# Performance work log

Hardware: AMD Instinct MI355X
Metric: run time of the kernel (lower is better)

The kernel has to match this reference:

```python
import jax, jax.numpy as jnp
import numpy as np

N_NODES = 100000
N_EDGES = 3200000
IN_DIM, HID_DIM, OUT_DIM = 128, 64, 2


def setup_inputs() -> dict:
    key = jax.random.key(0)
    k1, k2, k3, k4 = jax.random.split(key, 4)
    x = jax.random.normal(k1, (N_NODES, IN_DIM), dtype=jnp.float32)
    edge_index = jax.random.randint(k2, (2, N_EDGES), 0, N_NODES, dtype=jnp.int64)
    # GCNConv weights (glorot-style scale) and zero biases
    W1 = jax.random.normal(k3, (IN_DIM, HID_DIM), dtype=jnp.float32) / np.sqrt(IN_DIM)
    b1 = jnp.zeros((HID_DIM,), dtype=jnp.float32)
    W2 = jax.random.normal(k4, (HID_DIM, OUT_DIM), dtype=jnp.float32) / np.sqrt(HID_DIM)
    b2 = jnp.zeros((OUT_DIM,), dtype=jnp.float32)
    return {"x": x, "edge_index": edge_index, "W1": W1, "b1": b1, "W2": W2, "b2": b2}


def _gcn_norm(edge_index, num_nodes):
    # PyG GCNConv default: add self-loops, symmetric normalization deg^-1/2.
    loops = jnp.arange(num_nodes, dtype=edge_index.dtype)
    src = jnp.concatenate([edge_index[0], loops])  # [E+N]
    dst = jnp.concatenate([edge_index[1], loops])  # [E+N]
    deg = jax.ops.segment_sum(jnp.ones_like(dst, dtype=jnp.float32), dst,
                              num_segments=num_nodes)  # in-degree incl. self-loop
    dinv = jnp.where(deg > 0, jax.lax.rsqrt(deg), 0.0)
    norm = dinv[src] * dinv[dst]  # [E+N]
    return src, dst, norm


def _gcn_conv(h, W, b, src, dst, norm, num_nodes):
    h = h @ W                              # dense transform first (smaller dim)
    msg = h[src] * norm[:, None]           # gather + scale: [E+N, d]
    out = jax.ops.segment_sum(msg, dst, num_segments=num_nodes)  # scatter-add
    return out + b


def reference(x, edge_index, W1, b1, W2, b2):
    n = x.shape[0]
    src, dst, norm = _gcn_norm(edge_index, n)
    h = _gcn_conv(x, W1, b1, src, dst, norm, n)
    h = jax.nn.relu(h)
    return _gcn_conv(h, W2, b2, src, dst, norm, n)
```

## Files before the change

kernel.cpp:

```cpp
#include <hip/hip_runtime.h>
#include <hip/hip_bf16.h>


#define N_NODES 100000
#define IN_DIM 128
#define HID_DIM 64
#define OUT_DIM 2
#define NB 391
#define BCAP 12288
#define CROUNDS 12
#define CHUNK 8192

typedef short bf16x8 __attribute__((ext_vector_type(8)));
typedef float f32x4 __attribute__((ext_vector_type(4)));

__device__ __forceinline__ unsigned short f2bf(float x) {
    unsigned int u = __float_as_uint(x);
    unsigned int r = (u + 0x7FFFu + ((u >> 16) & 1u)) >> 16;
    return (unsigned short)r;
}
__device__ __forceinline__ float bflo(unsigned int u) { return __uint_as_float(u << 16); }
__device__ __forceinline__ float bfhi(unsigned int u) { return __uint_as_float(u & 0xFFFF0000u); }
__device__ __forceinline__ float4 unplo(uint4 r) {
    return make_float4(bflo(r.x), bflo(r.y), bflo(r.z), bflo(r.w));
}
__device__ __forceinline__ float4 unphi(uint4 r) {
    return make_float4(bfhi(r.x), bfhi(r.y), bfhi(r.z), bfhi(r.w));
}
__device__ __forceinline__ float4 f4add(float4 a, float4 v) {
    return make_float4(a.x + v.x, a.y + v.y, a.z + v.z, a.w + v.w);
}
__device__ __forceinline__ float4 f4fma(float m, float4 v, float4 a) {
    return make_float4(fmaf(m, v.x, a.x), fmaf(m, v.y, a.y),
                       fmaf(m, v.z, a.z), fmaf(m, v.w, a.w));
}
__device__ __forceinline__ int wave_incl_scan(int v, int laneid) {
#pragma unroll
    for (int off = 1; off < 64; off <<= 1) {
        int u = __shfl_up(v, off);
        if (laneid >= off) v += u;
    }
    return v;
}

__global__ __launch_bounds__(512) void part_kernel(const int* __restrict__ ei,
                                                   int* __restrict__ gCursor,
                                                   int* __restrict__ part, int E) {
    __shared__ int hist[512], lrow[512], gbase[512], lcur[512];
    __shared__ int lpk[CHUNK];
    __shared__ short lbkt[CHUNK];
    __shared__ int wsum[8], wofs[8];
    const int t = threadIdx.x;
    const int lane = t & 63, wv = t >> 6;
    const int base = blockIdx.x * CHUNK;
    const int cntC = min(CHUNK, E - base);

    hist[t] = 0;
    __syncthreads();

    int s[16], d[16];
    bool val[16];
    if (base + CHUNK <= E) {
#pragma unroll
        for (int i = 0; i < 4; ++i) {
            int4 sv = ((const int4*)(ei + base))[t + i * 512];
            int4 dv = ((const int4*)(ei + E + base))[t + i * 512];
            s[i * 4 + 0] = sv.x; s[i * 4 + 1] = sv.y; s[i * 4 + 2] = sv.z; s[i * 4 + 3] = sv.w;
            d[i * 4 + 0] = dv.x; d[i * 4 + 1] = dv.y; d[i * 4 + 2] = dv.z; d[i * 4 + 3] = dv.w;
            val[i * 4 + 0] = val[i * 4 + 1] = val[i * 4 + 2] = val[i * 4 + 3] = true;
        }
    } else {
#pragma unroll
        for (int i = 0; i < 16; ++i) {
            int e = base + t + i * 512;
            val[i] = (e < E);
            if (val[i]) {
                s[i] = ei[e];
                d[i] = ei[E + e];
            }
        }
    }
#pragma unroll
    for (int i = 0; i < 16; ++i)
        if (val[i]) atomicAdd(&hist[d[i] >> 8], 1);
    __syncthreads();

    int v = hist[t];
    int inc = wave_incl_scan(v, lane);
    if (lane == 63) wsum[wv] = inc;
    __syncthreads();
    if (t < 64) {
        int w = (t < 8) ? wsum[t] : 0;
        int wi = wave_incl_scan(w, t);
        if (t < 8) wofs[t] = wi - w;
    }
    __syncthreads();
    int excl = inc - v + wofs[wv];
    if (t < NB && v > 0) {
        int old = atomicAdd(&gCursor[t], v);
        gbase[t] = t * BCAP + old;
    }
    lcur[t] = excl;
    lrow[t] = excl;
    __syncthreads();

#pragma unroll
    for (int i = 0; i < 16; ++i) {
        if (val[i]) {
            int b = d[i] >> 8;
            int pos = atomicAdd(&lcur[b], 1);
            lpk[pos] = s[i] | ((d[i] & 255) << 20);
            lbkt[pos] = (short)b;
        }
    }
    __syncthreads();

    for (int i = t; i < cntC; i += 512) {
        int b = lbkt[i];
        int g = gbase[b] + (i - lrow[b]);
        if (g < (b + 1) * BCAP)
            part[g] = lpk[i];
    }
}

__global__ __launch_bounds__(1024) void csr_kernel(const int* __restrict__ part,
                                                   const int* __restrict__ gCursor,
                                                   int* __restrict__ cnt,
                                                   float* __restrict__ dinv,
                                                   int* __restrict__ rowptr,
                                                   int* __restrict__ csr_src, int n) {
    __shared__ int wcnt[16][256];
    __shared__ int wsum[4], wofs[4];
    const int b = blockIdx.x, t = threadIdx.x;
    const int lane = t & 63, wv = t >> 6;
    const int start = b * BCAP;
    const int count = min(gCursor[b], BCAP);

    for (int i = t; i < 16 * 256; i += 1024) ((int*)wcnt)[i] = 0;
    __syncthreads();

    int pk[CROUNDS];
    bool val[CROUNDS];
#pragma unroll
    for (int k = 0; k < CROUNDS; ++k) {
        int i = t + k * 1024;
        val[k] = (i < count);
        pk[k] = val[k] ? part[start + i] : 0;
        if (val[k]) atomicAdd(&wcnt[wv][(pk[k] >> 20) & 255], 1);
    }
    __syncthreads();

    int v = 0;
    if (t < 256) {
        int sum = 0;
#pragma unroll
        for (int w = 0; w < 16; ++w) sum += wcnt[w][t];
        v = sum;
    }
    int inc = 0;
    if (t < 256) {
        inc = wave_incl_scan(v, lane);
        if (lane == 63) wsum[wv] = inc;
    }
    __syncthreads();
    if (t < 64) {
        int w = (t < 4) ? wsum[t] : 0;
        int wi = wave_incl_scan(w, t);
        if (t < 4) wofs[t] = wi - w;
    }
    __syncthreads();
    if (t < 256) {
        int excl = inc - v + wofs[wv];
        int node = (b << 8) + t;
        if (node < n) {
            cnt[node] = v;
            dinv[node] = rsqrtf((float)v + 1.0f);
            rowptr[node] = start + excl;
        }
        int run = excl;
#pragma unroll
        for (int w = 0; w < 16; ++w) {
            int c = wcnt[w][t];
            wcnt[w][t] = run;
            run += c;
        }
    }
    __syncthreads();

#pragma unroll
    for (int k = 0; k < CROUNDS; ++k) {
        if (val[k]) {
            int pos = atomicAdd(&wcnt[wv][(pk[k] >> 20) & 255], 1);
            csr_src[start + pos] = pk[k] & 0xFFFFF;
        }
    }
}

__global__ __launch_bounds__(256) void gemm1_kernel(const float* __restrict__ x,
                                                    const float* __restrict__ W1,
                                                    const float* __restrict__ dinv,
                                                    unsigned short* __restrict__ hsb, int n) {
    __shared__ unsigned short sX[64 * 136];
    __shared__ unsigned short sW[64 * 136];
    const int tid = threadIdx.x;
    const int rbase = blockIdx.x * 64;

    for (int i = tid; i < 2048; i += 256) {
        int k = i >> 4, cq = (i & 15) << 2;
        float4 v = ((const float4*)W1)[i];
        sW[(cq + 0) * 136 + k] = f2bf(v.x);
        sW[(cq + 1) * 136 + k] = f2bf(v.y);
        sW[(cq + 2) * 136 + k] = f2bf(v.z);
        sW[(cq + 3) * 136 + k] = f2bf(v.w);
    }
    for (int i = tid; i < 2048; i += 256) {
        int r = i >> 5, kq = (i & 31) << 2;
        int gr = rbase + r;
        float4 v = make_float4(0.f, 0.f, 0.f, 0.f);
        if (gr < n) v = ((const float4*)x)[gr * 32 + (i & 31)];
        ushort4 u;
        u.x = f2bf(v.x); u.y = f2bf(v.y); u.z = f2bf(v.z); u.w = f2bf(v.w);
        *(ushort4*)&sX[r * 136 + kq] = u;
    }
    __syncthreads();

    const int wave = tid >> 6, lane = tid & 63;
    const int quad = lane >> 4, l16 = lane & 15;
    const int rowoff = wave * 16;

    f32x4 acc[4];
#pragma unroll
    for (int t = 0; t < 4; ++t) acc[t] = (f32x4){0.f, 0.f, 0.f, 0.f};

#pragma unroll
    for (int k0 = 0; k0 < 128; k0 += 32) {
        bf16x8 a = *(const bf16x8*)&sX[(rowoff + l16) * 136 + k0 + quad * 8];
#pragma unroll
        for (int t = 0; t < 4; ++t) {
            bf16x8 b = *(const bf16x8*)&sW[(t * 16 + l16) * 136 + k0 + quad * 8];
            acc[t] = __builtin_amdgcn_mfma_f32_16x16x32_bf16(a, b, acc[t], 0, 0, 0);
        }
    }

#pragma unroll
    for (int r = 0; r < 4; ++r) {
        int grow = rbase + rowoff + quad * 4 + r;
        if (grow < n) {
            float di = dinv[grow];
#pragma unroll
            for (int t = 0; t < 4; ++t)
                hsb[grow * HID_DIM + t * 16 + l16] = f2bf(acc[t][r] * di);
        }
    }
}

__global__ __launch_bounds__(256) void agg1_kernel(const int* __restrict__ rowptr,
                                                   const int* __restrict__ cnt,
                                                   const int* __restrict__ csr_src,
                                                   const unsigned short* __restrict__ hsb,
                                                   const float* __restrict__ dinv,
                                                   const float* __restrict__ b1,
                                                   const float* __restrict__ W2,
                                                   float* __restrict__ hs2, int n) {
    int node = blockIdx.x * 4 + (threadIdx.x >> 6);
    if (node >= n) return;
    int lane = threadIdx.x & 63;
    int g = lane >> 3;
    int l = lane & 7;
    int start = rowptr[node];
    int deg = cnt[node];

    float4 alo = make_float4(0.f, 0.f, 0.f, 0.f);
    float4 ahi = make_float4(0.f, 0.f, 0.f, 0.f);
    int s0 = (g      < deg) ? csr_src[start + g]      : 0;
    int s1 = (g +  8 < deg) ? csr_src[start + g +  8] : 0;
    int s2 = (g + 16 < deg) ? csr_src[start + g + 16] : 0;
    int s3 = (g + 24 < deg) ? csr_src[start + g + 24] : 0;
    for (int j = g; j < deg; j += 32) {
        int p0 = (j + 32 < deg) ? csr_src[start + j + 32] : 0;
        int p1 = (j + 40 < deg) ? csr_src[start + j + 40] : 0;
        int p2 = (j + 48 < deg) ? csr_src[start + j + 48] : 0;
        int p3 = (j + 56 < deg) ? csr_src[start + j + 56] : 0;
        uint4 r0 = *(const uint4*)&hsb[(unsigned)s0 * HID_DIM + l * 8];
        uint4 r1 = *(const uint4*)&hsb[(unsigned)s1 * HID_DIM + l * 8];
        uint4 r2 = *(const uint4*)&hsb[(unsigned)s2 * HID_DIM + l * 8];
        uint4 r3 = *(const uint4*)&hsb[(unsigned)s3 * HID_DIM + l * 8];
        float m1 = (j +  8 < deg) ? 1.0f : 0.0f;
        float m2 = (j + 16 < deg) ? 1.0f : 0.0f;
        float m3 = (j + 24 < deg) ? 1.0f : 0.0f;
        alo = f4add(alo, unplo(r0));      ahi = f4add(ahi, unphi(r0));
        alo = f4fma(m1, unplo(r1), alo);  ahi = f4fma(m1, unphi(r1), ahi);
        alo = f4fma(m2, unplo(r2), alo);  ahi = f4fma(m2, unphi(r2), ahi);
        alo = f4fma(m3, unplo(r3), alo);  ahi = f4fma(m3, unphi(r3), ahi);
        s0 = p0; s1 = p1; s2 = p2; s3 = p3;
    }

    float a[8];
    a[0] = alo.x; a[1] = ahi.x; a[2] = alo.y; a[3] = ahi.y;
    a[4] = alo.z; a[5] = ahi.z; a[6] = alo.w; a[7] = ahi.w;

#pragma unroll
    for (int off = 8; off <= 32; off <<= 1) {
#pragma unroll
        for (int i = 0; i < 8; ++i) a[i] += __shfl_xor(a[i], off);
    }

    {
        uint4 raw = *(const uint4*)&hsb[(unsigned)node * HID_DIM + l * 8];
        a[0] += bflo(raw.x); a[1] += bfhi(raw.x);
        a[2] += bflo(raw.y); a[3] += bfhi(raw.y);
        a[4] += bflo(raw.z); a[5] += bfhi(raw.z);
        a[6] += bflo(raw.w); a[7] += bfhi(raw.w);
    }

    float di = dinv[node];
    float4 bb0 = *(const float4*)&b1[l * 8];
    float4 bb1 = *(const float4*)&b1[l * 8 + 4];
    float t0 = fmaxf(fmaf(di, a[0], bb0.x), 0.0f);
    float t1 = fmaxf(fmaf(di, a[1], bb0.y), 0.0f);
    float t2 = fmaxf(fmaf(di, a[2], bb0.z), 0.0f);
    float t3 = fmaxf(fmaf(di, a[3], bb0.w), 0.0f);
    float t4 = fmaxf(fmaf(di, a[4], bb1.x), 0.0f);
    float t5 = fmaxf(fmaf(di, a[5], bb1.y), 0.0f);
    float t6 = fmaxf(fmaf(di, a[6], bb1.z), 0.0f);
    float t7 = fmaxf(fmaf(di, a[7], bb1.w), 0.0f);

    float4 w0 = *(const float4*)&W2[l * 16];
    float4 w1 = *(const float4*)&W2[l * 16 + 4];
    float4 w2 = *(const float4*)&W2[l * 16 + 8];
    float4 w3 = *(const float4*)&W2[l * 16 + 12];
    float p0 = t0 * w0.x + t1 * w0.z + t2 * w1.x + t3 * w1.z
             + t4 * w2.x + t5 * w2.z + t6 * w3.x + t7 * w3.z;
    float p1 = t0 * w0.y + t1 * w0.w + t2 * w1.y + t3 * w1.w
             + t4 * w2.y + t5 * w2.w + t6 * w3.y + t7 * w3.w;
    p0 += __shfl_xor(p0, 1);  p1 += __shfl_xor(p1, 1);
    p0 += __shfl_xor(p0, 2);  p1 += __shfl_xor(p1, 2);
    p0 += __shfl_xor(p0, 4);  p1 += __shfl_xor(p1, 4);

    if (lane == 0) {
        hs2[node * OUT_DIM + 0] = di * p0;
        hs2[node * OUT_DIM + 1] = di * p1;
    }
}

__global__ __launch_bounds__(256) void agg2_kernel(const int* __restrict__ rowptr,
                                                   const int* __restrict__ cnt,
                                                   const int* __restrict__ csr_src,
                                                   const float* __restrict__ hs2,
                                                   const float* __restrict__ dinv,
                                                   const float* __restrict__ b2,
                                                   float* __restrict__ out, int n) {
    int node = blockIdx.x * 8 + (threadIdx.x >> 5);
    if (node >= n) return;
    int lane = threadIdx.x & 31;
    int start = rowptr[node];
    int deg = cnt[node];

    float a0 = 0.0f, a1 = 0.0f;
    for (int j = lane; j < deg; j += 32) {
        int s = csr_src[start + j];
        float2 v = *(const float2*)&hs2[s * OUT_DIM];
        a0 += v.x;
        a1 += v.y;
    }
#pragma unroll
    for (int off = 16; off > 0; off >>= 1) {
        a0 += __shfl_xor(a0, off);
        a1 += __shfl_xor(a1, off);
    }
    if (lane == 0) {
        float di = dinv[node];
        float2 self = *(const float2*)&hs2[node * OUT_DIM];
        out[node * OUT_DIM + 0] = di * (a0 + self.x) + b2[0];
        out[node * OUT_DIM + 1] = di * (a1 + self.y) + b2[1];
    }
}

extern "C" void kernel_launch(void* const* d_in, const int* in_sizes, int n_in,
                              void* d_out, int out_size, void* d_ws, size_t ws_size,
                              hipStream_t stream) {
    const float* x  = (const float*)d_in[0];
    const int*   ei = (const int*)d_in[1];
    const float* W1 = (const float*)d_in[2];
    const float* b1 = (const float*)d_in[3];
    const float* W2 = (const float*)d_in[4];
    const float* b2 = (const float*)d_in[5];
    float* out = (float*)d_out;

    const int n = N_NODES;
    const int E = in_sizes[1] / 2;

    char* ws = (char*)d_ws;
    int*   gCursor = (int*)  (ws + 0);
    int*   cnt     = (int*)  (ws + (1u << 20));
    float* dinv    = (float*)(ws + (2u << 20));
    int*   rowptr  = (int*)  (ws + (3u << 20));
    float* hs2     = (float*)(ws + (4u << 20));
    int*   part    = (int*)  (ws + (5u << 20));
    unsigned short* hsb = (unsigned short*)(ws + (5u << 20));
    int*   csr_src = (int*)  (ws + (25u << 20));

    hipMemsetAsync(gCursor, 0, NB * sizeof(int), stream);

    part_kernel<<<(E + CHUNK - 1) / CHUNK, 512, 0, stream>>>(ei, gCursor, part, E);
    csr_kernel<<<NB, 1024, 0, stream>>>(part, gCursor, cnt, dinv, rowptr, csr_src, n);

    gemm1_kernel<<<(n + 63) / 64, 256, 0, stream>>>(x, W1, dinv, hsb, n);
    agg1_kernel<<<(n + 3) / 4, 256, 0, stream>>>(rowptr, cnt, csr_src, hsb, dinv, b1, W2, hs2, n);
    agg2_kernel<<<(n + 7) / 8, 256, 0, stream>>>(rowptr, cnt, csr_src, hs2, dinv, b2, out, n);
}
```

Measured before the change: 241.1 us.

## Fuse CSR local sort into layer-1 aggregation, shrink buckets to 128 nodes

```diff
diff --git a/kernel.cpp b/kernel.cpp
--- a/kernel.cpp
+++ b/kernel.cpp
@@ -6,9 +6,8 @@
 #define IN_DIM 128
 #define HID_DIM 64
 #define OUT_DIM 2
-#define NB 391
-#define BCAP 12288
-#define CROUNDS 12
+#define NB 782
+#define BCAP 5120
 #define CHUNK 8192
 
 typedef short bf16x8 __attribute__((ext_vector_type(8)));
@@ -43,13 +42,13 @@
     return v;
 }
 
-__global__ __launch_bounds__(512) void part_kernel(const int* __restrict__ ei,
-                                                   int* __restrict__ gCursor,
-                                                   int* __restrict__ part, int E) {
-    __shared__ int hist[512], lrow[512], gbase[512], lcur[512];
+__global__ __launch_bounds__(1024) void part_kernel(const int* __restrict__ ei,
+                                                    int* __restrict__ gCursor,
+                                                    int* __restrict__ part, int E) {
+    __shared__ int hist[1024], lrow[1024], gbase[1024], lcur[1024];
     __shared__ int lpk[CHUNK];
     __shared__ short lbkt[CHUNK];
-    __shared__ int wsum[8], wofs[8];
+    __shared__ int wsum[16], wofs[16];
     const int t = threadIdx.x;
     const int lane = t & 63, wv = t >> 6;
     const int base = blockIdx.x * CHUNK;
@@ -58,21 +57,21 @@
     hist[t] = 0;
     __syncthreads();
 
-    int s[16], d[16];
-    bool val[16];
+    int s[8], d[8];
+    bool val[8];
     if (base + CHUNK <= E) {
 #pragma unroll
-        for (int i = 0; i < 4; ++i) {
-            int4 sv = ((const int4*)(ei + base))[t + i * 512];
-            int4 dv = ((const int4*)(ei + E + base))[t + i * 512];
+        for (int i = 0; i < 2; ++i) {
+            int4 sv = ((const int4*)(ei + base))[t + i * 1024];
+            int4 dv = ((const int4*)(ei + E + base))[t + i * 1024];
             s[i * 4 + 0] = sv.x; s[i * 4 + 1] = sv.y; s[i * 4 + 2] = sv.z; s[i * 4 + 3] = sv.w;
             d[i * 4 + 0] = dv.x; d[i * 4 + 1] = dv.y; d[i * 4 + 2] = dv.z; d[i * 4 + 3] = dv.w;
             val[i * 4 + 0] = val[i * 4 + 1] = val[i * 4 + 2] = val[i * 4 + 3] = true;
         }
     } else {
 #pragma unroll
-        for (int i = 0; i < 16; ++i) {
-            int e = base + t + i * 512;
+        for (int i = 0; i < 8; ++i) {
+            int e = base + t + i * 1024;
             val[i] = (e < E);
             if (val[i]) {
                 s[i] = ei[e];
@@ -81,8 +80,8 @@
         }
     }
 #pragma unroll
-    for (int i = 0; i < 16; ++i)
-        if (val[i]) atomicAdd(&hist[d[i] >> 8], 1);
+    for (int i = 0; i < 8; ++i)
+        if (val[i]) atomicAdd(&hist[d[i] >> 7], 1);
     __syncthreads();
 
     int v = hist[t];
@@ -90,9 +89,9 @@
     if (lane == 63) wsum[wv] = inc;
     __syncthreads();
     if (t < 64) {
-        int w = (t < 8) ? wsum[t] : 0;
+        int w = (t < 16) ? wsum[t] : 0;
         int wi = wave_incl_scan(w, t);
-        if (t < 8) wofs[t] = wi - w;
+        if (t < 16) wofs[t] = wi - w;
     }
     __syncthreads();
     int excl = inc - v + wofs[wv];
@@ -105,17 +104,17 @@
     __syncthreads();
 
 #pragma unroll
-    for (int i = 0; i < 16; ++i) {
+    for (int i = 0; i < 8; ++i) {
         if (val[i]) {
-            int b = d[i] >> 8;
+            int b = d[i] >> 7;
             int pos = atomicAdd(&lcur[b], 1);
-            lpk[pos] = s[i] | ((d[i] & 255) << 20);
+            lpk[pos] = s[i] | ((d[i] & 127) << 20);
             lbkt[pos] = (short)b;
         }
     }
     __syncthreads();
 
-    for (int i = t; i < cntC; i += 512) {
+    for (int i = t; i < cntC; i += 1024) {
         int b = lbkt[i];
         int g = gbase[b] + (i - lrow[b]);
         if (g < (b + 1) * BCAP)
@@ -123,77 +122,20 @@
     }
 }
 
-__global__ __launch_bounds__(1024) void csr_kernel(const int* __restrict__ part,
+__global__ __launch_bounds__(256) void degs_kernel(const int* __restrict__ part,
                                                    const int* __restrict__ gCursor,
-                                                   int* __restrict__ cnt,
-                                                   float* __restrict__ dinv,
-                                                   int* __restrict__ rowptr,
-                                                   int* __restrict__ csr_src, int n) {
-    __shared__ int wcnt[16][256];
-    __shared__ int wsum[4], wofs[4];
+                                                   float* __restrict__ dinv, int n) {
+    __shared__ int lcnt[128];
     const int b = blockIdx.x, t = threadIdx.x;
-    const int lane = t & 63, wv = t >> 6;
     const int start = b * BCAP;
     const int count = min(gCursor[b], BCAP);
-
-    for (int i = t; i < 16 * 256; i += 1024) ((int*)wcnt)[i] = 0;
-    __syncthreads();
-
-    int pk[CROUNDS];
-    bool val[CROUNDS];
-#pragma unroll
-    for (int k = 0; k < CROUNDS; ++k) {
-        int i = t + k * 1024;
-        val[k] = (i < count);
-        pk[k] = val[k] ? part[start + i] : 0;
-        if (val[k]) atomicAdd(&wcnt[wv][(pk[k] >> 20) & 255], 1);
-    }
-    __syncthreads();
-
-    int v = 0;
-    if (t < 256) {
-        int sum = 0;
-#pragma unroll
-        for (int w = 0; w < 16; ++w) sum += wcnt[w][t];
-        v = sum;
-    }
-    int inc = 0;
-    if (t < 256) {
-        inc = wave_incl_scan(v, lane);
-        if (lane == 63) wsum[wv] = inc;
-    }
-    __syncthreads();
-    if (t < 64) {
-        int w = (t < 4) ? wsum[t] : 0;
-        int wi = wave_incl_scan(w, t);
-        if (t < 4) wofs[t] = wi - w;
-    }
-    __syncthreads();
-    if (t < 256) {
-        int excl = inc - v + wofs[wv];
-        int node = (b << 8) + t;
-        if (node < n) {
-            cnt[node] = v;
-            dinv[node] = rsqrtf((float)v + 1.0f);
-            rowptr[node] = start + excl;
-        }
-        int run = excl;
-#pragma unroll
-        for (int w = 0; w < 16; ++w) {
-            int c = wcnt[w][t];
-            wcnt[w][t] = run;
-            run += c;
-        }
-    }
-    __syncthreads();
-
-#pragma unroll
-    for (int k = 0; k < CROUNDS; ++k) {
-        if (val[k]) {
-            int pos = atomicAdd(&wcnt[wv][(pk[k] >> 20) & 255], 1);
-            csr_src[start + pos] = pk[k] & 0xFFFFF;
-        }
-    }
+    if (t < 128) lcnt[t] = 0;
+    __syncthreads();
+    for (int i = t; i < count; i += 256)
+        atomicAdd(&lcnt[(part[start + i] >> 20) & 127], 1);
+    __syncthreads();
+    int node = (b << 7) + t;
+    if (t < 128 && node < n) dinv[node] = rsqrtf((float)lcnt[t] + 1.0f);
 }
 
 __global__ __launch_bounds__(256) void gemm1_kernel(const float* __restrict__ x,
@@ -254,92 +196,154 @@
     }
 }
 
-__global__ __launch_bounds__(256) void agg1_kernel(const int* __restrict__ rowptr,
-                                                   const int* __restrict__ cnt,
-                                                   const int* __restrict__ csr_src,
-                                                   const unsigned short* __restrict__ hsb,
-                                                   const float* __restrict__ dinv,
-                                                   const float* __restrict__ b1,
-                                                   const float* __restrict__ W2,
-                                                   float* __restrict__ hs2, int n) {
-    int node = blockIdx.x * 4 + (threadIdx.x >> 6);
-    if (node >= n) return;
-    int lane = threadIdx.x & 63;
-    int g = lane >> 3;
-    int l = lane & 7;
-    int start = rowptr[node];
-    int deg = cnt[node];
-
-    float4 alo = make_float4(0.f, 0.f, 0.f, 0.f);
-    float4 ahi = make_float4(0.f, 0.f, 0.f, 0.f);
-    int s0 = (g      < deg) ? csr_src[start + g]      : 0;
-    int s1 = (g +  8 < deg) ? csr_src[start + g +  8] : 0;
-    int s2 = (g + 16 < deg) ? csr_src[start + g + 16] : 0;
-    int s3 = (g + 24 < deg) ? csr_src[start + g + 24] : 0;
-    for (int j = g; j < deg; j += 32) {
-        int p0 = (j + 32 < deg) ? csr_src[start + j + 32] : 0;
-        int p1 = (j + 40 < deg) ? csr_src[start + j + 40] : 0;
-        int p2 = (j + 48 < deg) ? csr_src[start + j + 48] : 0;
-        int p3 = (j + 56 < deg) ? csr_src[start + j + 56] : 0;
-        uint4 r0 = *(const uint4*)&hsb[(unsigned)s0 * HID_DIM + l * 8];
-        uint4 r1 = *(const uint4*)&hsb[(unsigned)s1 * HID_DIM + l * 8];
-        uint4 r2 = *(const uint4*)&hsb[(unsigned)s2 * HID_DIM + l * 8];
-        uint4 r3 = *(const uint4*)&hsb[(unsigned)s3 * HID_DIM + l * 8];
-        float m1 = (j +  8 < deg) ? 1.0f : 0.0f;
-        float m2 = (j + 16 < deg) ? 1.0f : 0.0f;
-        float m3 = (j + 24 < deg) ? 1.0f : 0.0f;
-        alo = f4add(alo, unplo(r0));      ahi = f4add(ahi, unphi(r0));
-        alo = f4fma(m1, unplo(r1), alo);  ahi = f4fma(m1, unphi(r1), ahi);
-        alo = f4fma(m2, unplo(r2), alo);  ahi = f4fma(m2, unphi(r2), ahi);
-        alo = f4fma(m3, unplo(r3), alo);  ahi = f4fma(m3, unphi(r3), ahi);
-        s0 = p0; s1 = p1; s2 = p2; s3 = p3;
-    }
-
-    float a[8];
-    a[0] = alo.x; a[1] = ahi.x; a[2] = alo.y; a[3] = ahi.y;
-    a[4] = alo.z; a[5] = ahi.z; a[6] = alo.w; a[7] = ahi.w;
-
-#pragma unroll
-    for (int off = 8; off <= 32; off <<= 1) {
-#pragma unroll
-        for (int i = 0; i < 8; ++i) a[i] += __shfl_xor(a[i], off);
-    }
-
-    {
-        uint4 raw = *(const uint4*)&hsb[(unsigned)node * HID_DIM + l * 8];
-        a[0] += bflo(raw.x); a[1] += bfhi(raw.x);
-        a[2] += bflo(raw.y); a[3] += bfhi(raw.y);
-        a[4] += bflo(raw.z); a[5] += bfhi(raw.z);
-        a[6] += bflo(raw.w); a[7] += bfhi(raw.w);
-    }
-
-    float di = dinv[node];
-    float4 bb0 = *(const float4*)&b1[l * 8];
-    float4 bb1 = *(const float4*)&b1[l * 8 + 4];
-    float t0 = fmaxf(fmaf(di, a[0], bb0.x), 0.0f);
-    float t1 = fmaxf(fmaf(di, a[1], bb0.y), 0.0f);
-    float t2 = fmaxf(fmaf(di, a[2], bb0.z), 0.0f);
-    float t3 = fmaxf(fmaf(di, a[3], bb0.w), 0.0f);
-    float t4 = fmaxf(fmaf(di, a[4], bb1.x), 0.0f);
-    float t5 = fmaxf(fmaf(di, a[5], bb1.y), 0.0f);
-    float t6 = fmaxf(fmaf(di, a[6], bb1.z), 0.0f);
-    float t7 = fmaxf(fmaf(di, a[7], bb1.w), 0.0f);
-
-    float4 w0 = *(const float4*)&W2[l * 16];
-    float4 w1 = *(const float4*)&W2[l * 16 + 4];
-    float4 w2 = *(const float4*)&W2[l * 16 + 8];
-    float4 w3 = *(const float4*)&W2[l * 16 + 12];
-    float p0 = t0 * w0.x + t1 * w0.z + t2 * w1.x + t3 * w1.z
-             + t4 * w2.x + t5 * w2.z + t6 * w3.x + t7 * w3.z;
-    float p1 = t0 * w0.y + t1 * w0.w + t2 * w1.y + t3 * w1.w
-             + t4 * w2.y + t5 * w2.w + t6 * w3.y + t7 * w3.w;
-    p0 += __shfl_xor(p0, 1);  p1 += __shfl_xor(p1, 1);
-    p0 += __shfl_xor(p0, 2);  p1 += __shfl_xor(p1, 2);
-    p0 += __shfl_xor(p0, 4);  p1 += __shfl_xor(p1, 4);
-
-    if (lane == 0) {
-        hs2[node * OUT_DIM + 0] = di * p0;
-        hs2[node * OUT_DIM + 1] = di * p1;
+__global__ __launch_bounds__(512) void aggsort_kernel(const int* __restrict__ part,
+                                                      const int* __restrict__ gCursor,
+                                                      const unsigned short* __restrict__ hsb,
+                                                      const float* __restrict__ dinv,
+                                                      const float* __restrict__ b1,
+                                                      const float* __restrict__ W2,
+                                                      int* __restrict__ cnt,
+                                                      int* __restrict__ rowptr,
+                                                      int* __restrict__ csr_src,
+                                                      float* __restrict__ hs2, int n) {
+    __shared__ int epk[BCAP];
+    __shared__ int sl[BCAP];
+    __shared__ int wcnt[8][128];
+    __shared__ int lrow[128], lcnt[128];
+    __shared__ int wsum[2];
+    const int b = blockIdx.x, t = threadIdx.x;
+    const int lane = t & 63, wv = t >> 6;
+    const int start = b * BCAP;
+    const int count = min(gCursor[b], BCAP);
+
+    for (int i = t; i < 8 * 128; i += 512) ((int*)wcnt)[i] = 0;
+    __syncthreads();
+
+    for (int i = t; i < count; i += 512) {
+        int p = part[start + i];
+        epk[i] = p;
+        atomicAdd(&wcnt[wv][(p >> 20) & 127], 1);
+    }
+    __syncthreads();
+
+    int v = 0, inc = 0;
+    if (t < 128) {
+        int sum = 0;
+#pragma unroll
+        for (int w = 0; w < 8; ++w) sum += wcnt[w][t];
+        v = sum;
+        inc = wave_incl_scan(v, lane);
+        if (lane == 63) wsum[t >> 6] = inc;
+    }
+    __syncthreads();
+    if (t < 128) {
+        int excl = inc - v + ((t >> 6) ? wsum[0] : 0);
+        int node = (b << 7) + t;
+        if (node < n) {
+            cnt[node] = v;
+            rowptr[node] = start + excl;
+        }
+        lcnt[t] = v;
+        lrow[t] = excl;
+        int run = excl;
+#pragma unroll
+        for (int w = 0; w < 8; ++w) {
+            int c = wcnt[w][t];
+            wcnt[w][t] = run;
+            run += c;
+        }
+    }
+    __syncthreads();
+
+    for (int i = t; i < count; i += 512) {
+        int p = epk[i];
+        int pos = atomicAdd(&wcnt[wv][(p >> 20) & 127], 1);
+        sl[pos] = p & 0xFFFFF;
+    }
+    __syncthreads();
+
+    for (int i = t; i < count; i += 512) csr_src[start + i] = sl[i];
+
+    const int g = lane >> 3;
+    const int l = lane & 7;
+    const float4 bb0 = *(const float4*)&b1[l * 8];
+    const float4 bb1 = *(const float4*)&b1[l * 8 + 4];
+    const float4 w0 = *(const float4*)&W2[l * 16];
+    const float4 w1 = *(const float4*)&W2[l * 16 + 4];
+    const float4 w2 = *(const float4*)&W2[l * 16 + 8];
+    const float4 w3 = *(const float4*)&W2[l * 16 + 12];
+
+    for (int nd = wv * 16; nd < wv * 16 + 16; ++nd) {
+        int gnode = (b << 7) + nd;
+        if (gnode >= n) break;
+        int st = lrow[nd];
+        int deg = lcnt[nd];
+
+        float4 alo = make_float4(0.f, 0.f, 0.f, 0.f);
+        float4 ahi = make_float4(0.f, 0.f, 0.f, 0.f);
+        int s0 = (g      < deg) ? sl[st + g]      : 0;
+        int s1 = (g +  8 < deg) ? sl[st + g +  8] : 0;
+        int s2 = (g + 16 < deg) ? sl[st + g + 16] : 0;
+        int s3 = (g + 24 < deg) ? sl[st + g + 24] : 0;
+        for (int j = g; j < deg; j += 32) {
+            int p0 = (j + 32 < deg) ? sl[st + j + 32] : 0;
+            int p1 = (j + 40 < deg) ? sl[st + j + 40] : 0;
+            int p2 = (j + 48 < deg) ? sl[st + j + 48] : 0;
+            int p3 = (j + 56 < deg) ? sl[st + j + 56] : 0;
+            uint4 r0 = *(const uint4*)&hsb[(unsigned)s0 * HID_DIM + l * 8];
+            uint4 r1 = *(const uint4*)&hsb[(unsigned)s1 * HID_DIM + l * 8];
+            uint4 r2 = *(const uint4*)&hsb[(unsigned)s2 * HID_DIM + l * 8];
+            uint4 r3 = *(const uint4*)&hsb[(unsigned)s3 * HID_DIM + l * 8];
+            float m1 = (j +  8 < deg) ? 1.0f : 0.0f;
+            float m2 = (j + 16 < deg) ? 1.0f : 0.0f;
+            float m3 = (j + 24 < deg) ? 1.0f : 0.0f;
+            alo = f4add(alo, unplo(r0));      ahi = f4add(ahi, unphi(r0));
+            alo = f4fma(m1, unplo(r1), alo);  ahi = f4fma(m1, unphi(r1), ahi);
+            alo = f4fma(m2, unplo(r2), alo);  ahi = f4fma(m2, unphi(r2), ahi);
+            alo = f4fma(m3, unplo(r3), alo);  ahi = f4fma(m3, unphi(r3), ahi);
+            s0 = p0; s1 = p1; s2 = p2; s3 = p3;
+        }
+
+        float a[8];
+        a[0] = alo.x; a[1] = ahi.x; a[2] = alo.y; a[3] = ahi.y;
+        a[4] = alo.z; a[5] = ahi.z; a[6] = alo.w; a[7] = ahi.w;
+
+#pragma unroll
+        for (int off = 8; off <= 32; off <<= 1) {
+#pragma unroll
+            for (int i = 0; i < 8; ++i) a[i] += __shfl_xor(a[i], off);
+        }
+
+        {
+            uint4 raw = *(const uint4*)&hsb[(unsigned)gnode * HID_DIM + l * 8];
+            a[0] += bflo(raw.x); a[1] += bfhi(raw.x);
+            a[2] += bflo(raw.y); a[3] += bfhi(raw.y);
+            a[4] += bflo(raw.z); a[5] += bfhi(raw.z);
+            a[6] += bflo(raw.w); a[7] += bfhi(raw.w);
+        }
+
+        float di = dinv[gnode];
+        float t0 = fmaxf(fmaf(di, a[0], bb0.x), 0.0f);
+        float t1 = fmaxf(fmaf(di, a[1], bb0.y), 0.0f);
+        float t2 = fmaxf(fmaf(di, a[2], bb0.z), 0.0f);
+        float t3 = fmaxf(fmaf(di, a[3], bb0.w), 0.0f);
+        float t4 = fmaxf(fmaf(di, a[4], bb1.x), 0.0f);
+        float t5 = fmaxf(fmaf(di, a[5], bb1.y), 0.0f);
+        float t6 = fmaxf(fmaf(di, a[6], bb1.z), 0.0f);
+        float t7 = fmaxf(fmaf(di, a[7], bb1.w), 0.0f);
+
+        float p0 = t0 * w0.x + t1 * w0.z + t2 * w1.x + t3 * w1.z
+                 + t4 * w2.x + t5 * w2.z + t6 * w3.x + t7 * w3.z;
+        float p1 = t0 * w0.y + t1 * w0.w + t2 * w1.y + t3 * w1.w
+                 + t4 * w2.y + t5 * w2.w + t6 * w3.y + t7 * w3.w;
+        p0 += __shfl_xor(p0, 1);  p1 += __shfl_xor(p1, 1);
+        p0 += __shfl_xor(p0, 2);  p1 += __shfl_xor(p1, 2);
+        p0 += __shfl_xor(p0, 4);  p1 += __shfl_xor(p1, 4);
+
+        if (lane == 0) {
+            hs2[gnode * OUT_DIM + 0] = di * p0;
+            hs2[gnode * OUT_DIM + 1] = di * p1;
+        }
     }
 }
 
@@ -397,15 +401,16 @@
     int*   rowptr  = (int*)  (ws + (3u << 20));
     float* hs2     = (float*)(ws + (4u << 20));
     int*   part    = (int*)  (ws + (5u << 20));
-    unsigned short* hsb = (unsigned short*)(ws + (5u << 20));
-    int*   csr_src = (int*)  (ws + (25u << 20));
+    int*   csr_src = (int*)  (ws + (22u << 20));
+    unsigned short* hsb = (unsigned short*)(ws + (39u << 20));
 
     hipMemsetAsync(gCursor, 0, NB * sizeof(int), stream);
 
-    part_kernel<<<(E + CHUNK - 1) / CHUNK, 512, 0, stream>>>(ei, gCursor, part, E);
-    csr_kernel<<<NB, 1024, 0, stream>>>(part, gCursor, cnt, dinv, rowptr, csr_src, n);
+    part_kernel<<<(E + CHUNK - 1) / CHUNK, 1024, 0, stream>>>(ei, gCursor, part, E);
+    degs_kernel<<<NB, 256, 0, stream>>>(part, gCursor, dinv, n);
 
     gemm1_kernel<<<(n + 63) / 64, 256, 0, stream>>>(x, W1, dinv, hsb, n);
-    agg1_kernel<<<(n + 3) / 4, 256, 0, stream>>>(rowptr, cnt, csr_src, hsb, dinv, b1, W2, hs2, n);
+    aggsort_kernel<<<NB, 512, 0, stream>>>(part, gCursor, hsb, dinv, b1, W2,
+                                           cnt, rowptr, csr_src, hs2, n);
     agg2_kernel<<<(n + 7) / 8, 256, 0, stream>>>(rowptr, cnt, csr_src, hs2, dinv, b2, out, n);
 }
```

Result: no change. 243.6 us (+1.1%).
